# Optimization experiments

Measured on AMD Instinct MI355X. Metric: run time of the kernel, lower is better.

Reference implementation:

```python
import jax, jax.numpy as jnp
import numpy as np

N = 50000      # nodes
NE = 10000     # hyperedges
NNZ = 600000   # incidence pairs
DIN = 128
DOUT = 128
ALPHA_RES = 0.5  # module's residual mixing coefficient


def _glorot(key, shape):
    fan_in, fan_out = shape[1], shape[0]
    lim = float(np.sqrt(6.0 / (fan_in + fan_out)))
    return jax.random.uniform(key, shape, jnp.float32, -lim, lim)


def setup_inputs() -> dict:
    key = jax.random.key(0)
    ks = jax.random.split(key, 9)
    X = jax.random.normal(ks[0], (N, DIN), jnp.float32)
    X0 = jax.random.normal(ks[1], (N, DIN), jnp.float32)
    vertex = jax.random.randint(ks[2], (NNZ,), 0, N)
    edges = jax.random.randint(ks[3], (NNZ,), 0, NE)
    alpha = jax.random.uniform(ks[4], (NNZ,), jnp.float32)
    # single-layer MLPs -> plain Linear weights (out, in) + bias
    W1_w = _glorot(ks[5], (DOUT, DIN))
    W1_b = jnp.zeros((DOUT,), jnp.float32)
    W2_w = _glorot(ks[6], (DOUT, DIN + DOUT))
    W2_b = jnp.zeros((DOUT,), jnp.float32)
    W_w = _glorot(ks[7], (DOUT, DOUT))
    W_b = jnp.zeros((DOUT,), jnp.float32)
    return {"X": X, "vertex": vertex, "edges": edges, "X0": X0, "alpha": alpha,
            "W1_w": W1_w, "W1_b": W1_b, "W2_w": W2_w, "W2_b": W2_b,
            "W_w": W_w, "W_b": W_b}


def reference(X, vertex, edges, X0, alpha, W1_w, W1_b, W2_w, W2_b, W_w, W_b):
    a = alpha[:, None]                                   # [nnz,1]
    # vertex -> edge: gather W1(X) rows, weight, scatter-add over hyperedges
    Xw1 = X @ W1_w.T + W1_b                              # [N, dout]
    Xve = Xw1[vertex] * a                                # [nnz, dout]
    Xe = jax.ops.segment_sum(Xve, edges, num_segments=NE)  # [NE, dout]
    # edge -> vertex: gather edge feats, concat with raw vertex feats, W2, scatter-add
    Xev = jnp.concatenate([X[vertex], Xe[edges]], axis=-1)  # [nnz, din+dout]
    Xev = (Xev @ W2_w.T + W2_b) * a                      # [nnz, dout]
    Xv = jax.ops.segment_sum(Xev, vertex, num_segments=N)  # [N, dout]
    Xr = (1.0 - ALPHA_RES) * Xv + ALPHA_RES * X0         # residual mix
    return Xr @ W_w.T + W_b
```

## Files before the change

kernel.cpp:

```cpp
#include <hip/hip_runtime.h>

#define NV   50000
#define NEV  10000
#define NNZV 600000
#define DIM  128

#define NBKE 157
#define NBKV 196
#define NCB  293
#define CH2  2048
#define SCAP 7680

#define BPACK_OFF 0
#define WP_OFF    24576
#define BA_OFF    40960
#define A_OFF     41216
#define B_OFF     91264
#define T_OFF     101312
#define XEBF_OFF  1381312
#define BCNTE_OFF 2021312
#define BOFFE_OFF 2021568
#define BCNTV_OFF 2021824
#define BOFFV_OFF 2022080
#define OFFE_OFF  2031328
#define CURE_OFF  2041344
#define OFFV_OFF  2101376
#define CURV_OFF  2151392
#define PV_OFF    2201920
#define PE_OUT_FLOAT_OFF 3200000

typedef __attribute__((ext_vector_type(8))) short bf16x8;
typedef __attribute__((ext_vector_type(4))) float f32x4;

__device__ __forceinline__ unsigned short f2bf(float x){
  unsigned u = __float_as_uint(x);
  u += 0x7fffu + ((u >> 16) & 1u);
  return (unsigned short)(u >> 16);
}
__device__ __forceinline__ float bf2f(unsigned short h){
  return __uint_as_float((unsigned)h << 16);
}

__global__ __launch_bounds__(128) void prep1(
        const float* __restrict__ W2w, const float* __restrict__ W2b,
        const float* __restrict__ Ww, float* __restrict__ ws){
  int b = blockIdx.x, o = threadIdx.x;
  if (b < 256){
    float s;
    if (b < 128){
      float acc = 0.f;
      for (int m = 0; m < 128; ++m) acc += Ww[o*128 + m] * W2w[m*256 + b];
      s = 0.5f * acc;
    } else {
      s = 0.5f * Ww[o*128 + (b - 128)];
    }
    int ks = b >> 5, g = (b >> 3) & 3, j = b & 7;
    int ct = o >> 4, lo = o & 15;
    unsigned short* Bp = (unsigned short*)(ws + BPACK_OFF);
    Bp[((size_t)((ks*8 + ct)*64 + g*16 + lo))*8 + j] = f2bf(s);
  } else if (b < 384){
    int m = b - 256;
    float acc = 0.f;
    for (int j = 0; j < 128; ++j) acc += Ww[o*128 + j] * W2w[j*256 + 128 + m];
    ws[T_OFF + m*128 + o] = 0.5f * acc;
  } else if (b == 384){
    float acc = 0.f;
    for (int m = 0; m < 128; ++m) acc += Ww[o*128 + m] * W2b[m];
    ws[BA_OFF + o] = 0.5f * acc;
  } else {
    int* z = (int*)(ws + BCNTE_OFF);
    int base = (b - 385)*256;
    z[base + o] = 0; z[base + 128 + o] = 0;
  }
}

__global__ __launch_bounds__(128) void prep2(
        const float* __restrict__ W1w, const float* __restrict__ W1b,
        float* __restrict__ ws){
  int b = blockIdx.x, o = threadIdx.x;
  const float* C2t = ws + T_OFF;
  if (b < 128){
    float acc = 0.f;
    for (int m = 0; m < 128; ++m) acc += W1w[m*128 + b] * C2t[m*128 + o];
    ws[WP_OFF + b*128 + o] = acc;
  } else {
    float acc = 0.f;
    for (int m = 0; m < 128; ++m) acc += W1b[m] * C2t[m*128 + o];
    ws[BA_OFF + 128 + o] = acc;
  }
}

__global__ __launch_bounds__(256) void count_tobf16(
        const int* __restrict__ vertex, const int* __restrict__ edges,
        const float* __restrict__ X,
        int* __restrict__ bcntE, int* __restrict__ bcntV,
        unsigned short* __restrict__ Xbf){
  int b = blockIdx.x, t = threadIdx.x;
  __shared__ int hE[256], hV[256];
  if (b < NCB){
    hE[t] = 0; hV[t] = 0;
    __syncthreads();
    int i0 = b * 2048;
    #pragma unroll
    for (int r = 0; r < 8; ++r){
      int i = i0 + r*256 + t;
      if (i < NNZV){
        atomicAdd(&hE[edges[i]  >> 6], 1);
        atomicAdd(&hV[vertex[i] >> 8], 1);
      }
    }
    __syncthreads();
    if (hE[t]) atomicAdd(bcntE + t, hE[t]);
    if (hV[t]) atomicAdd(bcntV + t, hV[t]);
  } else {
    int i = (b - NCB)*256 + t;
    if (i < NV*DIM/8){
      float4 v0 = ((const float4*)X)[(size_t)i*2];
      float4 v1 = ((const float4*)X)[(size_t)i*2 + 1];
      ushort4 h0, h1;
      h0.x=f2bf(v0.x); h0.y=f2bf(v0.y); h0.z=f2bf(v0.z); h0.w=f2bf(v0.w);
      h1.x=f2bf(v1.x); h1.y=f2bf(v1.y); h1.z=f2bf(v1.z); h1.w=f2bf(v1.w);
      ((ushort4*)Xbf)[(size_t)i*2]     = h0;
      ((ushort4*)Xbf)[(size_t)i*2 + 1] = h1;
    }
  }
}

__global__ __launch_bounds__(256) void scan_buckets(
        const int* __restrict__ bcntE, const int* __restrict__ bcntV,
        int* __restrict__ bOffE, int* __restrict__ bOffV,
        int* __restrict__ bcurE, int* __restrict__ bcurV,
        int* __restrict__ offE, int* __restrict__ offV){
  __shared__ int s[256];
  int t = threadIdx.x;
  int c = (t < NBKE) ? bcntE[t] : 0;
  s[t] = c; __syncthreads();
  for (int d = 1; d < 256; d <<= 1){
    int x = (t >= d) ? s[t-d] : 0;
    __syncthreads(); s[t] += x; __syncthreads();
  }
  if (t < NBKE){ bOffE[t] = s[t] - c; bcurE[t] = s[t] - c; }
  if (t == 0){ bOffE[NBKE] = NNZV; offE[NEV] = NNZV; }
  __syncthreads();
  int c2 = (t < NBKV) ? bcntV[t] : 0;
  s[t] = c2; __syncthreads();
  for (int d = 1; d < 256; d <<= 1){
    int x = (t >= d) ? s[t-d] : 0;
    __syncthreads(); s[t] += x; __syncthreads();
  }
  if (t < NBKV){ bOffV[t] = s[t] - c2; bcurV[t] = s[t] - c2; }
  if (t == 0){ bOffV[NBKV] = NNZV; offV[NV] = NNZV; }
}

__global__ __launch_bounds__(256) void fill_binned2(
        const int* __restrict__ vertex, const int* __restrict__ edges,
        const float* __restrict__ alpha,
        int* __restrict__ bcurE, int* __restrict__ bcurV,
        int2* __restrict__ PE, int2* __restrict__ PV){
  __shared__ int histE[256], lofsE[256], gbaseE[256], posE[256];
  __shared__ int histV[256], lofsV[256], gbaseV[256], posV[256];
  __shared__ int ss[256];
  __shared__ int2 stgE[CH2], stgV[CH2];
  int t = threadIdx.x;
  int i0 = blockIdx.x * CH2;
  histE[t] = 0; histV[t] = 0;
  __syncthreads();
  int pkE[8], pkV[8], pa[8];
  #pragma unroll
  for (int r = 0; r < 8; ++r){
    int i = i0 + r*256 + t;
    int pe = -1, pv = -1, ab = 0;
    if (i < NNZV){
      int v = vertex[i], e = edges[i];
      ab = __float_as_int(alpha[i]);
      pe = (e << 16) | v;
      pv = (v << 14) | e;
      atomicAdd(&histE[pe >> 22], 1);
      atomicAdd(&histV[pv >> 22], 1);
    }
    pkE[r] = pe; pkV[r] = pv; pa[r] = ab;
  }
  __syncthreads();
  int cE = histE[t];
  ss[t] = cE; __syncthreads();
  for (int d = 1; d < 256; d <<= 1){
    int x = (t >= d) ? ss[t-d] : 0;
    __syncthreads(); ss[t] += x; __syncthreads();
  }
  lofsE[t] = ss[t] - cE; posE[t] = ss[t] - cE;
  __syncthreads();
  int cV = histV[t];
  ss[t] = cV; __syncthreads();
  for (int d = 1; d < 256; d <<= 1){
    int x = (t >= d) ? ss[t-d] : 0;
    __syncthreads(); ss[t] += x; __syncthreads();
  }
  lofsV[t] = ss[t] - cV; posV[t] = ss[t] - cV;
  __syncthreads();
  #pragma unroll
  for (int r = 0; r < 8; ++r){
    if (pkE[r] != -1){
      int p = atomicAdd(&posE[pkE[r] >> 22], 1);
      stgE[p] = make_int2(pkE[r], pa[r]);
      int q = atomicAdd(&posV[pkV[r] >> 22], 1);
      stgV[q] = make_int2(pkV[r], pa[r]);
    }
  }
  __syncthreads();
  {
    int cnt = histE[t];
    gbaseE[t] = cnt ? atomicAdd(&bcurE[t], cnt) : 0;
    int cnt2 = histV[t];
    gbaseV[t] = cnt2 ? atomicAdd(&bcurV[t], cnt2) : 0;
  }
  __syncthreads();
  int total = min(CH2, NNZV - i0);
  for (int s = t; s < total; s += 256){
    int lo = 0, hi = NBKE - 1;
    while (lo < hi){ int mid = (lo + hi + 1) >> 1; if (lofsE[mid] <= s) lo = mid; else hi = mid - 1; }
    PE[gbaseE[lo] + (s - lofsE[lo])] = stgE[s];
    lo = 0; hi = NBKV - 1;
    while (lo < hi){ int mid = (lo + hi + 1) >> 1; if (lofsV[mid] <= s) lo = mid; else hi = mid - 1; }
    PV[gbaseV[lo] + (s - lofsV[lo])] = stgV[s];
  }
}

__global__ __launch_bounds__(256) void sort_bucket(
        int2* __restrict__ pairs, const int* __restrict__ bOff,
        int* __restrict__ off, float* __restrict__ sums,
        int2* __restrict__ bounce, int kpb, int shift, int nkeys){
  int b = blockIdx.x, t = threadIdx.x;
  int k0 = b * kpb;
  int r0 = bOff[b], r1 = bOff[b+1];
  int m = r1 - r0;
  __shared__ int hist[256], rnk[256], ssc[256];
  __shared__ int2 srt[SCAP];
  for (int q = t; q < kpb; q += 256) hist[q] = 0;
  __syncthreads();
  int px[30], py[30];
  #pragma unroll
  for (int r = 0; r < 30; ++r){
    int s = r*256 + t;
    int x = -1, y = 0;
    if (s < m && m <= SCAP){
      int2 p = pairs[r0 + s];
      x = p.x; y = p.y;
      atomicAdd(&hist[(x >> shift) - k0], 1);
    }
    px[r] = x; py[r] = y;
  }
  if (m > SCAP){
    for (int s = t; s < m; s += 256){
      int2 p = pairs[r0 + s];
      bounce[s] = p;
      atomicAdd(&hist[(p.x >> shift) - k0], 1);
    }
  }
  __syncthreads();
  int c = (t < kpb) ? hist[t] : 0;
  ssc[t] = c; __syncthreads();
  for (int d = 1; d < 256; d <<= 1){
    int x = (t >= d) ? ssc[t-d] : 0;
    __syncthreads(); ssc[t] += x; __syncthreads();
  }
  if (t < kpb){
    rnk[t] = ssc[t] - c;
    int k = k0 + t;
    if (k < nkeys) off[k] = r0 + ssc[t] - c;
  }
  __syncthreads();
  if (m <= SCAP){
    #pragma unroll
    for (int r = 0; r < 30; ++r){
      if (px[r] >= 0){
        int p = atomicAdd(&rnk[(px[r] >> shift) - k0], 1);
        srt[p] = make_int2(px[r], py[r]);
      }
    }
    __syncthreads();
    for (int s = t; s < m; s += 256) pairs[r0 + s] = srt[s];
    if (t < kpb){
      int k = k0 + t;
      if (k < nkeys){
        float sa = 0.f;
        int s0 = ssc[t] - hist[t], s1 = ssc[t];
        for (int s = s0; s < s1; ++s) sa += __int_as_float(srt[s].y);
        sums[k] = sa;
      }
    }
  } else {
    __syncthreads();
    for (int s = t; s < m; s += 256){
      int2 p = bounce[s];
      int q = atomicAdd(&rnk[(p.x >> shift) - k0], 1);
      pairs[r0 + q] = p;
    }
    __syncthreads();
    if (t < kpb){
      int k = k0 + t;
      if (k < nkeys){
        float sa = 0.f;
        int s0 = ssc[t] - hist[t], s1 = ssc[t];
        for (int s = s0; s < s1; ++s) sa += __int_as_float(pairs[r0 + s].y);
        sums[k] = sa;
      }
    }
  }
}

__global__ __launch_bounds__(256) void edge_reduce(
        const unsigned short* __restrict__ Xbf, const int* __restrict__ offE,
        const int2* __restrict__ PE, float* __restrict__ T){
  int w = threadIdx.x >> 6, l = threadIdx.x & 63;
  int e = blockIdx.x*4 + w;
  int s0 = offE[e], s1 = offE[e+1];
  float acc0 = 0.f, acc1 = 0.f;
  int j = s0;
  for (; j + 8 <= s1; j += 8){
    int2 p[8];
    #pragma unroll
    for (int q = 0; q < 8; ++q) p[q] = PE[j + q];
    float x0[8], x1[8];
    #pragma unroll
    for (int q = 0; q < 8; ++q){
      int v = (p[q].x & 0xFFFF) << 7;
      x0[q] = bf2f(Xbf[v + l]);
      x1[q] = bf2f(Xbf[v + 64 + l]);
    }
    #pragma unroll
    for (int q = 0; q < 8; ++q){
      float a = __int_as_float(p[q].y);
      acc0 += a * x0[q]; acc1 += a * x1[q];
    }
  }
  for (; j < s1; ++j){
    int2 p = PE[j];
    int v = (p.x & 0xFFFF) << 7;
    float a = __int_as_float(p.y);
    acc0 += a * bf2f(Xbf[v + l]);
    acc1 += a * bf2f(Xbf[v + 64 + l]);
  }
  size_t o = (size_t)e * DIM;
  T[o + l]      = acc0;
  T[o + 64 + l] = acc1;
}

__global__ __launch_bounds__(256) void gemm_ye(float* __restrict__ ws){
  __shared__ float Y[32][136];
  const float* T   = ws + T_OFF;
  const float* WP  = ws + WP_OFF;
  const float* Bs  = ws + B_OFF;
  const float* b1p = ws + BA_OFF + 128;
  unsigned short* Ye = (unsigned short*)(ws + XEBF_OFF);
  int n0 = blockIdx.x * 32;
  int tid = threadIdx.x;
  {
    int lr = tid >> 3, lj = tid & 7;
    int gn = n0 + lr; if (gn >= NEV) gn = NEV - 1;
    const float* src = T + (size_t)gn*DIM + lj*16;
    #pragma unroll
    for (int q = 0; q < 4; ++q)
      *(float4*)(&Y[lr][lj*16 + q*4]) = *(const float4*)(src + q*4);
  }
  __syncthreads();
  int rq = tid >> 5, cq = tid & 31;
  float acc[4][4];
  #pragma unroll
  for (int u=0;u<4;++u){ acc[u][0]=0;acc[u][1]=0;acc[u][2]=0;acc[u][3]=0; }
  const float* Crow = WP + cq*4;
  #pragma unroll 4
  for (int k = 0; k < 128; ++k){
    float4 c = *(const float4*)(Crow + (size_t)k*128);
    #pragma unroll
    for (int u = 0; u < 4; ++u){
      float y = Y[rq*4 + u][k];
      acc[u][0] += y*c.x; acc[u][1] += y*c.y; acc[u][2] += y*c.z; acc[u][3] += y*c.w;
    }
  }
  float4 b1v = *(const float4*)(b1p + cq*4);
  #pragma unroll
  for (int u = 0; u < 4; ++u){
    int e = n0 + rq*4 + u;
    if (e < NEV){
      float Bv = Bs[e];
      ushort4 h;
      h.x = f2bf(acc[u][0] + Bv*b1v.x); h.y = f2bf(acc[u][1] + Bv*b1v.y);
      h.z = f2bf(acc[u][2] + Bv*b1v.z); h.w = f2bf(acc[u][3] + Bv*b1v.w);
      *(ushort4*)(Ye + (size_t)e*DIM + cq*4) = h;
    }
  }
}

#define LDS_STRIDE 264

__global__ __launch_bounds__(256) void gemm_pq(
        const float* __restrict__ X, const float* __restrict__ X0,
        const float* __restrict__ Wb, const float* __restrict__ ws,
        float* __restrict__ R){
  __shared__ unsigned short At[64 * LDS_STRIDE];
  __shared__ float ArS[64];
  const float* Aa = ws + A_OFF;
  const float* bA = ws + BA_OFF;
  const unsigned short* Bpack = (const unsigned short*)(ws + BPACK_OFF);
  int r0 = blockIdx.x * 64;
  int t = threadIdx.x;
  if (t < 64){
    int gn = r0 + t; if (gn >= NV) gn = NV - 1;
    ArS[t] = Aa[gn];
  }
  __syncthreads();
  #pragma unroll
  for (int seg = 0; seg < 2; ++seg){
    const float* src = (seg == 0) ? X : X0;
    #pragma unroll
    for (int i = 0; i < 8; ++i){
      int idx = t + i*256;
      int row = idx >> 5;
      int c4  = idx & 31;
      int gn = r0 + row; if (gn >= NV) gn = NV - 1;
      float4 v = *(const float4*)(src + (size_t)gn*DIM + c4*4);
      if (seg == 0){
        float Ar = ArS[row];
        v.x *= Ar; v.y *= Ar; v.z *= Ar; v.w *= Ar;
      }
      ushort4 h;
      h.x = f2bf(v.x); h.y = f2bf(v.y); h.z = f2bf(v.z); h.w = f2bf(v.w);
      *(ushort4*)(&At[row*LDS_STRIDE + seg*128 + c4*4]) = h;
    }
  }
  __syncthreads();

  int w = t >> 6, l = t & 63;
  int m0 = w * 16;
  int lr = l & 15, lg = l >> 4;
  f32x4 acc[8];
  #pragma unroll
  for (int ct = 0; ct < 8; ++ct) acc[ct] = (f32x4){0.f,0.f,0.f,0.f};

  const unsigned short* arow = &At[(m0 + lr)*LDS_STRIDE + lg*8];
  #pragma unroll
  for (int ks = 0; ks < 8; ++ks){
    bf16x8 af = *(const bf16x8*)(arow + ks*32);
    const bf16x8* bp = (const bf16x8*)(Bpack) + (size_t)ks*8*64 + l;
    #pragma unroll
    for (int ct = 0; ct < 8; ++ct){
      bf16x8 bf = bp[ct*64];
      acc[ct] = __builtin_amdgcn_mfma_f32_16x16x32_bf16(af, bf, acc[ct], 0, 0, 0);
    }
  }

  #pragma unroll
  for (int ct = 0; ct < 8; ++ct){
    int o = ct*16 + lr;
    float ba = bA[o], wb = Wb[o];
    #pragma unroll
    for (int r = 0; r < 4; ++r){
      int lrow = m0 + lg*4 + r;
      int row = r0 + lrow;
      if (row < NV){
        float Av = ArS[lrow];
        R[(size_t)row*DIM + o] = acc[ct][r] + Av*ba + wb;
      }
    }
  }
}

__global__ __launch_bounds__(256) void vertex_fused(
        const unsigned short* __restrict__ Ye, const int* __restrict__ offV,
        const int2* __restrict__ PV, float* __restrict__ out){
  int w = threadIdx.x >> 6, l = threadIdx.x & 63;
  int v = blockIdx.x*4 + w;
  int s0 = offV[v], s1 = offV[v+1];
  float acc0 = 0.f, acc1 = 0.f;
  int j = s0;
  for (; j + 8 <= s1; j += 8){
    int2 p[8];
    #pragma unroll
    for (int q = 0; q < 8; ++q) p[q] = PV[j + q];
    float y0[8], y1[8];
    #pragma unroll
    for (int q = 0; q < 8; ++q){
      int e = (p[q].x & 0x3FFF) << 7;
      y0[q] = bf2f(Ye[e + l]);
      y1[q] = bf2f(Ye[e + 64 + l]);
    }
    #pragma unroll
    for (int q = 0; q < 8; ++q){
      float a = __int_as_float(p[q].y);
      acc0 += a * y0[q]; acc1 += a * y1[q];
    }
  }
  for (; j < s1; ++j){
    int2 p = PV[j];
    int e = (p.x & 0x3FFF) << 7;
    float a = __int_as_float(p.y);
    acc0 += a * bf2f(Ye[e + l]);
    acc1 += a * bf2f(Ye[e + 64 + l]);
  }
  size_t o = (size_t)v * DIM;
  out[o + l]      += acc0;
  out[o + 64 + l] += acc1;
}

extern "C" void kernel_launch(void* const* d_in, const int* in_sizes, int n_in,
                              void* d_out, int out_size, void* d_ws, size_t ws_size,
                              hipStream_t stream){
  const float* X    = (const float*)d_in[0];
  const int*  vertex= (const int*)  d_in[1];
  const int*  edges = (const int*)  d_in[2];
  const float* X0   = (const float*)d_in[3];
  const float* alpha= (const float*)d_in[4];
  const float* W1w  = (const float*)d_in[5];
  const float* W1b  = (const float*)d_in[6];
  const float* W2w  = (const float*)d_in[7];
  const float* W2b  = (const float*)d_in[8];
  const float* Ww   = (const float*)d_in[9];
  const float* Wb   = (const float*)d_in[10];
  float* out = (float*)d_out;
  float* ws  = (float*)d_ws;

  int* bcntE = (int*)(ws + BCNTE_OFF);
  int* bOffE = (int*)(ws + BOFFE_OFF);
  int* bcntV = (int*)(ws + BCNTV_OFF);
  int* bOffV = (int*)(ws + BOFFV_OFF);
  int* offE  = (int*)(ws + OFFE_OFF);
  int* bcurE = (int*)(ws + CURE_OFF);
  int* offV  = (int*)(ws + OFFV_OFF);
  int* bcurV = (int*)(ws + CURV_OFF);
  int2* PV   = (int2*)(ws + PV_OFF);
  int2* PE   = (int2*)(out + PE_OUT_FLOAT_OFF);
  int2* bounce = (int2*)(ws + T_OFF);
  unsigned short* Xbf = (unsigned short*)out;
  unsigned short* Ye  = (unsigned short*)(ws + XEBF_OFF);

  prep1        <<<389, 128, 0, stream>>>(W2w, W2b, Ww, ws);
  prep2        <<<129, 128, 0, stream>>>(W1w, W1b, ws);
  count_tobf16 <<<NCB + (NV*DIM/8 + 255)/256, 256, 0, stream>>>(vertex, edges, X,
                                                                bcntE, bcntV, Xbf);
  scan_buckets <<<1, 256, 0, stream>>>(bcntE, bcntV, bOffE, bOffV, bcurE, bcurV,
                                       offE, offV);
  fill_binned2 <<<(NNZV + CH2 - 1)/CH2, 256, 0, stream>>>(vertex, edges, alpha,
                                                          bcurE, bcurV, PE, PV);
  sort_bucket  <<<NBKE, 256, 0, stream>>>(PE, bOffE, offE, ws + B_OFF, bounce, 64,  16, NEV);
  sort_bucket  <<<NBKV, 256, 0, stream>>>(PV, bOffV, offV, ws + A_OFF, bounce, 256, 14, NV);
  edge_reduce  <<<NEV/4, 256, 0, stream>>>(Xbf, offE, PE, ws + T_OFF);
  gemm_ye      <<<(NEV + 31)/32, 256, 0, stream>>>(ws);
  gemm_pq      <<<(NV + 63)/64, 256, 0, stream>>>(X, X0, Wb, ws, out);
  vertex_fused <<<NV/4, 256, 0, stream>>>(Ye, offV, PV, out);
}
```

Measured before the change: 181.4 us.

## Use packed 32-bit bf16 gathers and drop LDS staging in gemm_pq

The edge_reduce and vertex_fused gathers now read two adjacent bf16 values per lane with one 32-bit load and write float2 pairs, replacing two separate 16-bit loads per row and two scalar stores. This halves the number of gather load instructions for the memory-bound scatter/gather phases. gemm_pq no longer stages X/X0 through LDS: each lane loads its own float4 pairs straight from global memory, scales and converts them into MFMA A fragments, which removes LDS traffic and both barriers. The trade-off is less coalesced global reads in gemm_pq, since each lane reads 32-byte pieces of different rows.

```diff
diff --git a/kernel.cpp b/kernel.cpp
--- a/kernel.cpp
+++ b/kernel.cpp
@@ -320,29 +320,30 @@
     int2 p[8];
     #pragma unroll
     for (int q = 0; q < 8; ++q) p[q] = PE[j + q];
-    float x0[8], x1[8];
+    float lo[8], hi[8];
     #pragma unroll
     for (int q = 0; q < 8; ++q){
       int v = (p[q].x & 0xFFFF) << 7;
-      x0[q] = bf2f(Xbf[v + l]);
-      x1[q] = bf2f(Xbf[v + 64 + l]);
+      unsigned xx = *(const unsigned*)(Xbf + v + 2*l);
+      lo[q] = bf2f((unsigned short)(xx & 0xFFFF));
+      hi[q] = bf2f((unsigned short)(xx >> 16));
     }
     #pragma unroll
     for (int q = 0; q < 8; ++q){
       float a = __int_as_float(p[q].y);
-      acc0 += a * x0[q]; acc1 += a * x1[q];
+      acc0 += a * lo[q]; acc1 += a * hi[q];
     }
   }
   for (; j < s1; ++j){
     int2 p = PE[j];
     int v = (p.x & 0xFFFF) << 7;
+    unsigned xx = *(const unsigned*)(Xbf + v + 2*l);
     float a = __int_as_float(p.y);
-    acc0 += a * bf2f(Xbf[v + l]);
-    acc1 += a * bf2f(Xbf[v + 64 + l]);
-  }
-  size_t o = (size_t)e * DIM;
-  T[o + l]      = acc0;
-  T[o + 64 + l] = acc1;
+    acc0 += a * bf2f((unsigned short)(xx & 0xFFFF));
+    acc1 += a * bf2f((unsigned short)(xx >> 16));
+  }
+  float2 o2; o2.x = acc0; o2.y = acc1;
+  *(float2*)(T + (size_t)e*DIM + 2*l) = o2;
 }
 
 __global__ __launch_bounds__(256) void gemm_ye(float* __restrict__ ws){
@@ -391,76 +392,58 @@
   }
 }
 
-#define LDS_STRIDE 264
-
 __global__ __launch_bounds__(256) void gemm_pq(
         const float* __restrict__ X, const float* __restrict__ X0,
         const float* __restrict__ Wb, const float* __restrict__ ws,
         float* __restrict__ R){
-  __shared__ unsigned short At[64 * LDS_STRIDE];
-  __shared__ float ArS[64];
   const float* Aa = ws + A_OFF;
   const float* bA = ws + BA_OFF;
   const unsigned short* Bpack = (const unsigned short*)(ws + BPACK_OFF);
-  int r0 = blockIdx.x * 64;
   int t = threadIdx.x;
-  if (t < 64){
-    int gn = r0 + t; if (gn >= NV) gn = NV - 1;
-    ArS[t] = Aa[gn];
-  }
-  __syncthreads();
-  #pragma unroll
-  for (int seg = 0; seg < 2; ++seg){
-    const float* src = (seg == 0) ? X : X0;
-    #pragma unroll
-    for (int i = 0; i < 8; ++i){
-      int idx = t + i*256;
-      int row = idx >> 5;
-      int c4  = idx & 31;
-      int gn = r0 + row; if (gn >= NV) gn = NV - 1;
-      float4 v = *(const float4*)(src + (size_t)gn*DIM + c4*4);
-      if (seg == 0){
-        float Ar = ArS[row];
-        v.x *= Ar; v.y *= Ar; v.z *= Ar; v.w *= Ar;
-      }
-      ushort4 h;
-      h.x = f2bf(v.x); h.y = f2bf(v.y); h.z = f2bf(v.z); h.w = f2bf(v.w);
-      *(ushort4*)(&At[row*LDS_STRIDE + seg*128 + c4*4]) = h;
-    }
-  }
-  __syncthreads();
-
   int w = t >> 6, l = t & 63;
-  int m0 = w * 16;
   int lr = l & 15, lg = l >> 4;
+  int r0 = blockIdx.x * 64 + w * 16;
+  int ar = r0 + lr; if (ar >= NV) ar = NV - 1;
+  float Ar = Aa[ar];
+  const float* xrow  = X  + (size_t)ar*DIM + lg*8;
+  const float* x0row = X0 + (size_t)ar*DIM + lg*8;
   f32x4 acc[8];
   #pragma unroll
   for (int ct = 0; ct < 8; ++ct) acc[ct] = (f32x4){0.f,0.f,0.f,0.f};
-
-  const unsigned short* arow = &At[(m0 + lr)*LDS_STRIDE + lg*8];
   #pragma unroll
   for (int ks = 0; ks < 8; ++ks){
-    bf16x8 af = *(const bf16x8*)(arow + ks*32);
+    const float* src = (ks < 4) ? (xrow + ks*32) : (x0row + (ks-4)*32);
+    float4 v0 = *(const float4*)(src);
+    float4 v1 = *(const float4*)(src + 4);
+    if (ks < 4){
+      v0.x*=Ar; v0.y*=Ar; v0.z*=Ar; v0.w*=Ar;
+      v1.x*=Ar; v1.y*=Ar; v1.z*=Ar; v1.w*=Ar;
+    }
+    bf16x8 af;
+    af[0]=(short)f2bf(v0.x); af[1]=(short)f2bf(v0.y);
+    af[2]=(short)f2bf(v0.z); af[3]=(short)f2bf(v0.w);
+    af[4]=(short)f2bf(v1.x); af[5]=(short)f2bf(v1.y);
+    af[6]=(short)f2bf(v1.z); af[7]=(short)f2bf(v1.w);
     const bf16x8* bp = (const bf16x8*)(Bpack) + (size_t)ks*8*64 + l;
     #pragma unroll
-    for (int ct = 0; ct < 8; ++ct){
-      bf16x8 bf = bp[ct*64];
-      acc[ct] = __builtin_amdgcn_mfma_f32_16x16x32_bf16(af, bf, acc[ct], 0, 0, 0);
-    }
-  }
-
+    for (int ct = 0; ct < 8; ++ct)
+      acc[ct] = __builtin_amdgcn_mfma_f32_16x16x32_bf16(af, bp[ct*64], acc[ct], 0, 0, 0);
+  }
+  float Av_[4];
+  #pragma unroll
+  for (int r = 0; r < 4; ++r){
+    int row = r0 + lg*4 + r;
+    Av_[r] = (row < NV) ? Aa[row] : 0.f;
+  }
   #pragma unroll
   for (int ct = 0; ct < 8; ++ct){
     int o = ct*16 + lr;
     float ba = bA[o], wb = Wb[o];
     #pragma unroll
     for (int r = 0; r < 4; ++r){
-      int lrow = m0 + lg*4 + r;
-      int row = r0 + lrow;
-      if (row < NV){
-        float Av = ArS[lrow];
-        R[(size_t)row*DIM + o] = acc[ct][r] + Av*ba + wb;
-      }
+      int row = r0 + lg*4 + r;
+      if (row < NV)
+        R[(size_t)row*DIM + o] = acc[ct][r] + Av_[r]*ba + wb;
     }
   }
 }
@@ -477,29 +460,32 @@
     int2 p[8];
     #pragma unroll
     for (int q = 0; q < 8; ++q) p[q] = PV[j + q];
-    float y0[8], y1[8];
+    float lo[8], hi[8];
     #pragma unroll
     for (int q = 0; q < 8; ++q){
       int e = (p[q].x & 0x3FFF) << 7;
-      y0[q] = bf2f(Ye[e + l]);
-      y1[q] = bf2f(Ye[e + 64 + l]);
+      unsigned yy = *(const unsigned*)(Ye + e + 2*l);
+      lo[q] = bf2f((unsigned short)(yy & 0xFFFF));
+      hi[q] = bf2f((unsigned short)(yy >> 16));
     }
     #pragma unroll
     for (int q = 0; q < 8; ++q){
       float a = __int_as_float(p[q].y);
-      acc0 += a * y0[q]; acc1 += a * y1[q];
+      acc0 += a * lo[q]; acc1 += a * hi[q];
     }
   }
   for (; j < s1; ++j){
     int2 p = PV[j];
     int e = (p.x & 0x3FFF) << 7;
+    unsigned yy = *(const unsigned*)(Ye + e + 2*l);
     float a = __int_as_float(p.y);
-    acc0 += a * bf2f(Ye[e + l]);
-    acc1 += a * bf2f(Ye[e + 64 + l]);
-  }
-  size_t o = (size_t)v * DIM;
-  out[o + l]      += acc0;
-  out[o + 64 + l] += acc1;
+    acc0 += a * bf2f((unsigned short)(yy & 0xFFFF));
+    acc1 += a * bf2f((unsigned short)(yy >> 16));
+  }
+  float* dst = out + (size_t)v*DIM + 2*l;
+  float2 cur = *(float2*)dst;
+  cur.x += acc0; cur.y += acc1;
+  *(float2*)dst = cur;
 }
 
 extern "C" void kernel_launch(void* const* d_in, const int* in_sizes, int n_in,
```

New measurement: 179.2 us, median of 2. No clear change (-1.2%).
